# Performance work log

Hardware: AMD Instinct MI355X
Metric: run time of the kernel (lower is better)

Reference implementation:

```python
import jax, jax.numpy as jnp
import numpy as np

N_ATOMS = 100000
N_BONDS = 400000
ATOM_FDIM = 133
BOND_FDIM = 147
HIDDEN = 300
DEPTH = 3


def setup_inputs() -> dict:
    key = jax.random.key(0)
    ks = jax.random.split(key, 10)
    f_atoms = jax.random.normal(ks[0], (N_ATOMS, ATOM_FDIM), dtype=jnp.float32)
    f_bonds = jax.random.normal(ks[1], (N_BONDS, BOND_FDIM), dtype=jnp.float32)
    b2a = jax.random.randint(ks[2], (N_BONDS,), 0, N_ATOMS)
    b2revb = jax.random.randint(ks[3], (N_BONDS,), 0, N_BONDS)
    s_i = 1.0 / np.sqrt(BOND_FDIM)
    s_h = 1.0 / np.sqrt(HIDDEN)
    s_o = 1.0 / np.sqrt(ATOM_FDIM + HIDDEN)
    Wi_w = jax.random.uniform(ks[4], (HIDDEN, BOND_FDIM), jnp.float32, -s_i, s_i)
    Wi_b = jax.random.uniform(ks[5], (HIDDEN,), jnp.float32, -s_i, s_i)
    Wh_w = jax.random.uniform(ks[6], (HIDDEN, HIDDEN), jnp.float32, -s_h, s_h)
    Wh_b = jax.random.uniform(ks[7], (HIDDEN,), jnp.float32, -s_h, s_h)
    Wo_w = jax.random.uniform(ks[8], (HIDDEN, ATOM_FDIM + HIDDEN), jnp.float32, -s_o, s_o)
    Wo_b = jax.random.uniform(ks[9], (HIDDEN,), jnp.float32, -s_o, s_o)
    return {"f_atoms": f_atoms, "f_bonds": f_bonds, "b2a": b2a, "b2revb": b2revb,
            "Wi_w": Wi_w, "Wi_b": Wi_b, "Wh_w": Wh_w, "Wh_b": Wh_b,
            "Wo_w": Wo_w, "Wo_b": Wo_b}


def reference(f_atoms, f_bonds, b2a, b2revb, Wi_w, Wi_b, Wh_w, Wh_b, Wo_w, Wo_b):
    n_atoms = f_atoms.shape[0]
    # initial bond messages: [n_bonds, hidden]
    H_bonds = jax.nn.relu(f_bonds @ Wi_w.T + Wi_b)
    dest = b2a[b2revb]  # destination atom of each directed bond
    for _ in range(DEPTH - 1):
        # scatter-add bond messages onto destination atoms
        sum_msgs = jax.ops.segment_sum(H_bonds, dest, num_segments=n_atoms)
        # gather back to bonds from source atoms, subtract reverse-bond message
        msgs = sum_msgs[b2a] - H_bonds[b2revb]
        H_bonds = jax.nn.relu(H_bonds + msgs @ Wh_w.T + Wh_b)
    sum_msgs = jax.ops.segment_sum(H_bonds, dest, num_segments=n_atoms)
    H_atoms = jax.nn.relu(jnp.concatenate([f_atoms, sum_msgs], axis=1) @ Wo_w.T + Wo_b)
    return (H_atoms, H_bonds)
```

## Files before the change

kernel.cpp:

```cpp
#include <hip/hip_runtime.h>
#include <hip/hip_bf16.h>

#define NB 400000
#define NA 100000
#define AFD 133
#define BFD 147
#define HID 300
#define NP  320
#define SMP 304
#define NT  98

typedef short short8 __attribute__((ext_vector_type(8)));
typedef float f32x4 __attribute__((ext_vector_type(4)));

__device__ __forceinline__ ushort f2b(float f) {
    union { float f; unsigned u; } v; v.f = f;
    unsigned r = v.u + 0x7fffu + ((v.u >> 16) & 1u);
    return (ushort)(r >> 16);
}
__device__ __forceinline__ float b2f(ushort u) {
    union { unsigned u; float f; } v; v.u = ((unsigned)u) << 16;
    return v.f;
}

#define GLDS(gp, lp) __builtin_amdgcn_global_load_lds( \
    (const __attribute__((address_space(1))) void*)(gp), \
    (__attribute__((address_space(3))) void*)(lp), 16, 0, 0)


__global__ void pad_w_k(const float* __restrict__ W, ushort* __restrict__ Wp,
                        int N, int K, int Kp) {
    int idx = blockIdx.x * 256 + threadIdx.x;
    if (idx >= NP * Kp) return;
    int n = idx / Kp, k = idx - n * Kp;
    int t = k >> 5, kk = k & 31;
    int g = (kk & 15) >> 2, slot = (kk & 3) + ((kk >> 4) << 2);
    int gp = g ^ ((n >> 1) & 3);
    ushort v = (n < N && k < K) ? f2b(W[n * K + k]) : (ushort)0;
    Wp[(size_t)t * 10240 + n * 32 + gp * 8 + slot] = v;
}

__global__ void dest_k(const int* __restrict__ b2a, const int* __restrict__ b2revb,
                       int* __restrict__ dest) {
    int b = blockIdx.x * 256 + threadIdx.x;
    if (b < NB) dest[b] = b2a[b2revb[b]];
}

__global__ void count_k(const int* __restrict__ dest, int* __restrict__ cnt) {
    int b = blockIdx.x * 256 + threadIdx.x;
    if (b < NB) atomicAdd(&cnt[dest[b]], 1);
}

__global__ void scanA_k(const int* __restrict__ cnt, int* __restrict__ tsum) {
    __shared__ int sm[256];
    const int tid = threadIdx.x;
    int base = blockIdx.x * 1024 + tid * 4;
    int s = 0;
#pragma unroll
    for (int j = 0; j < 4; ++j) { int i = base + j; if (i < NA) s += cnt[i]; }
    sm[tid] = s; __syncthreads();
    for (int o = 128; o > 0; o >>= 1) {
        if (tid < o) sm[tid] += sm[tid + o];
        __syncthreads();
    }
    if (tid == 0) tsum[blockIdx.x] = sm[0];
}

__global__ void scanB_k(const int* __restrict__ tsum, int* __restrict__ toff,
                        int* __restrict__ rs) {
    if (threadIdx.x == 0) {
        int run = 0;
        for (int t = 0; t < NT; ++t) { toff[t] = run; run += tsum[t]; }
        rs[NA] = run;
    }
}

__global__ void scanC_k(const int* __restrict__ cnt, const int* __restrict__ toff,
                        int* __restrict__ rs) {
    __shared__ int sm[256];
    const int tid = threadIdx.x;
    int base = blockIdx.x * 1024 + tid * 4;
    int v[4]; int s = 0;
#pragma unroll
    for (int j = 0; j < 4; ++j) {
        v[j] = (base + j < NA) ? cnt[base + j] : 0;
        s += v[j];
    }
    sm[tid] = s; __syncthreads();
    for (int o = 1; o < 256; o <<= 1) {
        int x = (tid >= o) ? sm[tid - o] : 0;
        __syncthreads();
        sm[tid] += x;
        __syncthreads();
    }
    int acc = sm[tid] - s + toff[blockIdx.x];
#pragma unroll
    for (int j = 0; j < 4; ++j) {
        if (base + j < NA) rs[base + j] = acc;
        acc += v[j];
    }
}

__global__ void scatter_k(const int* __restrict__ dest, const int* __restrict__ rs,
                          int* __restrict__ cur, int* __restrict__ bl) {
    int b = blockIdx.x * 256 + threadIdx.x;
    if (b >= NB) return;
    int a = dest[b];
    int pos = rs[a] + atomicAdd(&cur[a], 1);
    bl[pos] = b;
}

template<int MODE, bool OUTF>
__global__ __launch_bounds__(512) void gemm_k(
    const float* __restrict__ F1, const float* __restrict__ Sum,
    const ushort* __restrict__ HbIn,
    const int* __restrict__ b2a, const int* __restrict__ b2revb,
    const ushort* __restrict__ W, const float* __restrict__ bias,
    ushort* __restrict__ Cb, float* __restrict__ Cf, int M)
{
    constexpr int KP = (MODE == 0) ? 192 : (MODE == 1) ? 320 : 448;
    constexpr int TILES = KP / 32;
    static_assert(KP % 64 == 0 && TILES % 2 == 0, "XOR swizzle needs 128B-mult rows, even tiles");
    __shared__ ushort As[128 * KP];
    __shared__ ushort Bs[2][320 * 32];

    const int tid = threadIdx.x;
    const int w = tid >> 6, lane = tid & 63;
    const int wr = w >> 2, wc = w & 3;
    const int g = lane >> 4, lr = lane & 15;
    const int m0 = blockIdx.x * 128;

    {
        const int row = tid >> 2, q = tid & 3;
        int grow = m0 + row;
        if (MODE == 2 && grow >= M) grow = M - 1;
        const int axw = (row & 7) << 4;
        char* abase = (char*)As + (size_t)row * (KP * 2);
        const float* sp = nullptr; const ushort* hp = nullptr;
        if (MODE == 1) {
            sp = Sum + (size_t)b2a[grow] * SMP;
            hp = HbIn + (size_t)b2revb[grow] * NP;
        }
#pragma unroll
        for (int t = 0; t < TILES; ++t) {
            const int k0 = t * 32 + 4 * q, k1 = k0 + 16;
            ushort o[8];
            if (MODE == 0) {
                const float* src = F1 + (size_t)grow * BFD;
#pragma unroll
                for (int s = 0; s < 4; ++s) o[s]     = (k0 + s < BFD) ? f2b(src[k0 + s]) : (ushort)0;
#pragma unroll
                for (int s = 0; s < 4; ++s) o[4 + s] = (k1 + s < BFD) ? f2b(src[k1 + s]) : (ushort)0;
            } else if (MODE == 1) {
                float4 s0 = *(const float4*)(sp + k0);
                float4 s1 = (k1 < SMP) ? *(const float4*)(sp + k1)
                                       : make_float4(0.f, 0.f, 0.f, 0.f);
                ushort4 h0 = *(const ushort4*)(hp + k0);
                ushort4 h1 = *(const ushort4*)(hp + k1);
                o[0] = f2b(s0.x - b2f(h0.x)); o[1] = f2b(s0.y - b2f(h0.y));
                o[2] = f2b(s0.z - b2f(h0.z)); o[3] = f2b(s0.w - b2f(h0.w));
                o[4] = f2b(s1.x - b2f(h1.x)); o[5] = f2b(s1.y - b2f(h1.y));
                o[6] = f2b(s1.z - b2f(h1.z)); o[7] = f2b(s1.w - b2f(h1.w));
            } else {
#pragma unroll
                for (int s = 0; s < 8; ++s) {
                    int k = (s < 4) ? (k0 + s) : (k1 + s - 4);
                    float x = 0.f;
                    if (k < AFD) x = F1[(size_t)grow * AFD + k];
                    else if (k < AFD + HID) x = Sum[(size_t)grow * SMP + (k - AFD)];
                    o[s] = f2b(x);
                }
            }
            ushort* dst = (ushort*)(abase + ((t * 64 + q * 16) ^ axw));
            *(ushort4*)dst       = make_ushort4(o[0], o[1], o[2], o[3]);
            *(ushort4*)(dst + 4) = make_ushort4(o[4], o[5], o[6], o[7]);
        }
    }

    auto stageB = [&](int t, int buf) {
        const ushort* wt = W + (size_t)t * 10240;
        ushort* bs = &Bs[buf][0];
        GLDS(wt + (size_t)w * 512 + lane * 8,        bs + w * 512);
        GLDS(wt + (size_t)(w + 8) * 512 + lane * 8,  bs + (w + 8) * 512);
        if (w < 4)
            GLDS(wt + (size_t)(w + 16) * 512 + lane * 8, bs + (w + 16) * 512);
    };

    f32x4 acc[4][5];
#pragma unroll
    for (int mi = 0; mi < 4; ++mi)
#pragma unroll
        for (int ni = 0; ni < 5; ++ni) acc[mi][ni] = (f32x4){0.f, 0.f, 0.f, 0.f};

    stageB(0, 0);
    __syncthreads();

    const int raxw = (lr & 7) << 4;
    const int bswz = ((lr >> 1) & 3);
    for (int t = 0; t < TILES; ++t) {
        if (t + 1 < TILES) stageB(t + 1, (t + 1) & 1);
        const ushort* bs = &Bs[t & 1][0];
        short8 af[4];
#pragma unroll
        for (int mi = 0; mi < 4; ++mi) {
            const int r = wr * 64 + mi * 16 + lr;
            af[mi] = *(const short8*)((const char*)As + (size_t)r * (KP * 2)
                                      + ((t * 64 + g * 16) ^ raxw));
        }
#pragma unroll
        for (int ni = 0; ni < 5; ++ni) {
            const int c = wc * 80 + ni * 16 + lr;
            short8 bf = *(const short8*)&bs[c * 32 + ((g ^ bswz) << 3)];
#pragma unroll
            for (int mi = 0; mi < 4; ++mi)
                acc[mi][ni] = __builtin_amdgcn_mfma_f32_16x16x32_bf16(af[mi], bf, acc[mi][ni], 0, 0, 0);
        }
        __syncthreads();
    }

#pragma unroll
    for (int ni = 0; ni < 5; ++ni) {
        const int col = wc * 80 + ni * 16 + lr;
        const float bv = (col < HID) ? bias[col] : 0.f;
#pragma unroll
        for (int mi = 0; mi < 4; ++mi) {
            const int row0 = m0 + wr * 64 + mi * 16 + g * 4;
#pragma unroll
            for (int r = 0; r < 4; ++r) {
                const int row = row0 + r;
                float v = acc[mi][ni][r] + bv;
                if (MODE == 1) v += b2f(HbIn[(size_t)row * NP + col]);
                v = fmaxf(v, 0.f);
                if (MODE == 2) {
                    if (col < HID && row < M) Cf[(size_t)row * HID + col] = v;
                } else {
                    Cb[(size_t)row * NP + col] = f2b(v);
                    if (OUTF && col < HID) Cf[(size_t)row * HID + col] = v;
                }
            }
        }
    }
}

__global__ void seg_sum_csr_k(const ushort* __restrict__ Hb, const int* __restrict__ rs,
                              const int* __restrict__ bl, float* __restrict__ sum) {
    int idx = blockIdx.x * 256 + threadIdx.x;
    if (idx >= NA * 38) return;
    int a = idx / 38, c = (idx - a * 38) * 8;
    int s0 = rs[a], s1 = rs[a + 1];
    float acc[8] = {0.f, 0.f, 0.f, 0.f, 0.f, 0.f, 0.f, 0.f};
    for (int j = s0; j < s1; ++j) {
        const ushort* p = &Hb[(size_t)bl[j] * NP + c];
        ushort4 u0 = *(const ushort4*)p, u1 = *(const ushort4*)(p + 4);
        acc[0] += b2f(u0.x); acc[1] += b2f(u0.y);
        acc[2] += b2f(u0.z); acc[3] += b2f(u0.w);
        acc[4] += b2f(u1.x); acc[5] += b2f(u1.y);
        acc[6] += b2f(u1.z); acc[7] += b2f(u1.w);
    }
    float* dst = &sum[(size_t)a * SMP + c];
    *(float4*)dst       = make_float4(acc[0], acc[1], acc[2], acc[3]);
    *(float4*)(dst + 4) = make_float4(acc[4], acc[5], acc[6], acc[7]);
}

extern "C" void kernel_launch(void* const* d_in, const int* in_sizes, int n_in,
                              void* d_out, int out_size, void* d_ws, size_t ws_size,
                              hipStream_t stream) {
    const float* f_atoms = (const float*)d_in[0];
    const float* f_bonds = (const float*)d_in[1];
    const int*   b2a     = (const int*)d_in[2];
    const int*   b2revb  = (const int*)d_in[3];
    const float* Wi_w    = (const float*)d_in[4];
    const float* Wi_b    = (const float*)d_in[5];
    const float* Wh_w    = (const float*)d_in[6];
    const float* Wh_b    = (const float*)d_in[7];
    const float* Wo_w    = (const float*)d_in[8];
    const float* Wo_b    = (const float*)d_in[9];
    float* out = (float*)d_out;

    char* ws = (char*)d_ws;
    ushort* HbA  = (ushort*)ws;            ws += (size_t)NB * NP * 2;
    ushort* HbB  = (ushort*)ws;            ws += (size_t)NB * NP * 2;
    float*  sum  = (float*)ws;             ws += (size_t)NA * SMP * 4;
    int*    dest = (int*)ws;               ws += (size_t)NB * 4;
    ushort* Wp0  = (ushort*)ws;            ws += (size_t)6  * 10240 * 2;
    ushort* Wp1  = (ushort*)ws;            ws += (size_t)10 * 10240 * 2;
    ushort* Wp2  = (ushort*)ws;            ws += (size_t)14 * 10240 * 2;
    int*    cnt  = (int*)ws;               ws += (size_t)NA * 4;
    int*    cur  = (int*)ws;               ws += (size_t)NA * 4;
    int*    rs   = (int*)ws;               ws += (size_t)(NA + 1) * 4;
    int*    bl   = (int*)ws;               ws += (size_t)NB * 4;
    int*    tsum = (int*)ws;               ws += 128 * 4;
    int*    toff = (int*)ws;               ws += 128 * 4;
    float* Hatoms = out;
    float* Hbonds = out + (size_t)NA * HID;

    pad_w_k<<<(NP * 192 + 255) / 256, 256, 0, stream>>>(Wi_w, Wp0, HID, BFD, 192);
    pad_w_k<<<(NP * NP  + 255) / 256, 256, 0, stream>>>(Wh_w, Wp1, HID, HID, NP);
    pad_w_k<<<(NP * 448 + 255) / 256, 256, 0, stream>>>(Wo_w, Wp2, HID, AFD + HID, 448);
    dest_k<<<(NB + 255) / 256, 256, 0, stream>>>(b2a, b2revb, dest);
    hipMemsetAsync(cnt, 0, (size_t)NA * 4, stream);
    hipMemsetAsync(cur, 0, (size_t)NA * 4, stream);
    count_k<<<(NB + 255) / 256, 256, 0, stream>>>(dest, cnt);
    scanA_k<<<NT, 256, 0, stream>>>(cnt, tsum);
    scanB_k<<<1, 64, 0, stream>>>(tsum, toff, rs);
    scanC_k<<<NT, 256, 0, stream>>>(cnt, toff, rs);
    scatter_k<<<(NB + 255) / 256, 256, 0, stream>>>(dest, rs, cur, bl);

    gemm_k<0, false><<<NB / 128, 512, 0, stream>>>(
        f_bonds, nullptr, nullptr, nullptr, nullptr, Wp0, Wi_b, HbA, nullptr, NB);

    seg_sum_csr_k<<<(NA * 38 + 255) / 256, 256, 0, stream>>>(HbA, rs, bl, sum);
    gemm_k<1, false><<<NB / 128, 512, 0, stream>>>(
        nullptr, sum, HbA, b2a, b2revb, Wp1, Wh_b, HbB, nullptr, NB);

    seg_sum_csr_k<<<(NA * 38 + 255) / 256, 256, 0, stream>>>(HbB, rs, bl, sum);
    gemm_k<1, true><<<NB / 128, 512, 0, stream>>>(
        nullptr, sum, HbB, b2a, b2revb, Wp1, Wh_b, HbA, Hbonds, NB);

    seg_sum_csr_k<<<(NA * 38 + 255) / 256, 256, 0, stream>>>(HbA, rs, bl, sum);
    gemm_k<2, false><<<(NA + 127) / 128, 512, 0, stream>>>(
        f_atoms, sum, nullptr, nullptr, nullptr, Wp2, Wo_b, nullptr, Hatoms, NA);
}
```

Measured before the change: 1.808 ms.

## Apply Wh before message passing and stream A tiles via direct-to-LDS loads

Uses linearity so that Y = H·Whᵀ is computed first, then segment-summed and gathered (sum_msgs·W − H_rev·W) in a separate elementwise update kernel, instead of building the gathered message matrix inside the GEMM prologue. The new H GEMM reads its A operand with global_load_lds double buffering like B, removing the gather from the GEMM. The change adds an extra Y buffer, an extra bf16 SY round-trip and another launch per iteration. Bf16 rounding now happens at different points, which may change accuracy. The K-slot layout of the packed weights is also changed to contiguous groups of 8.

```diff
diff --git a/kernel.cpp b/kernel.cpp
--- a/kernel.cpp
+++ b/kernel.cpp
@@ -34,10 +34,15 @@
     if (idx >= NP * Kp) return;
     int n = idx / Kp, k = idx - n * Kp;
     int t = k >> 5, kk = k & 31;
-    int g = (kk & 15) >> 2, slot = (kk & 3) + ((kk >> 4) << 2);
+    int g = kk >> 3, s = kk & 7;
     int gp = g ^ ((n >> 1) & 3);
     ushort v = (n < N && k < K) ? f2b(W[n * K + k]) : (ushort)0;
-    Wp[(size_t)t * 10240 + n * 32 + gp * 8 + slot] = v;
+    Wp[(size_t)t * 10240 + n * 32 + gp * 8 + s] = v;
+}
+
+__global__ void pad_bias_k(const float* __restrict__ bh, float* __restrict__ bhp) {
+    int i = blockIdx.x * 256 + threadIdx.x;
+    if (i < NP) bhp[i] = (i < HID) ? bh[i] : 0.f;
 }
 
 __global__ void dest_k(const int* __restrict__ b2a, const int* __restrict__ b2revb,
@@ -110,17 +115,15 @@
     bl[pos] = b;
 }
 
-template<int MODE, bool OUTF>
+template<int MODE>
 __global__ __launch_bounds__(512) void gemm_k(
     const float* __restrict__ F1, const float* __restrict__ Sum,
-    const ushort* __restrict__ HbIn,
-    const int* __restrict__ b2a, const int* __restrict__ b2revb,
     const ushort* __restrict__ W, const float* __restrict__ bias,
     ushort* __restrict__ Cb, float* __restrict__ Cf, int M)
 {
-    constexpr int KP = (MODE == 0) ? 192 : (MODE == 1) ? 320 : 448;
+    constexpr int KP = (MODE == 0) ? 192 : 448;
     constexpr int TILES = KP / 32;
-    static_assert(KP % 64 == 0 && TILES % 2 == 0, "XOR swizzle needs 128B-mult rows, even tiles");
+    static_assert(KP % 64 == 0 && TILES % 2 == 0, "XOR swizzle needs 128B rows, even tiles");
     __shared__ ushort As[128 * KP];
     __shared__ ushort Bs[2][320 * 32];
 
@@ -136,38 +139,22 @@
         if (MODE == 2 && grow >= M) grow = M - 1;
         const int axw = (row & 7) << 4;
         char* abase = (char*)As + (size_t)row * (KP * 2);
-        const float* sp = nullptr; const ushort* hp = nullptr;
-        if (MODE == 1) {
-            sp = Sum + (size_t)b2a[grow] * SMP;
-            hp = HbIn + (size_t)b2revb[grow] * NP;
-        }
 #pragma unroll
         for (int t = 0; t < TILES; ++t) {
-            const int k0 = t * 32 + 4 * q, k1 = k0 + 16;
+            const int k0 = t * 32 + q * 8;
             ushort o[8];
             if (MODE == 0) {
                 const float* src = F1 + (size_t)grow * BFD;
 #pragma unroll
-                for (int s = 0; s < 4; ++s) o[s]     = (k0 + s < BFD) ? f2b(src[k0 + s]) : (ushort)0;
-#pragma unroll
-                for (int s = 0; s < 4; ++s) o[4 + s] = (k1 + s < BFD) ? f2b(src[k1 + s]) : (ushort)0;
-            } else if (MODE == 1) {
-                float4 s0 = *(const float4*)(sp + k0);
-                float4 s1 = (k1 < SMP) ? *(const float4*)(sp + k1)
-                                       : make_float4(0.f, 0.f, 0.f, 0.f);
-                ushort4 h0 = *(const ushort4*)(hp + k0);
-                ushort4 h1 = *(const ushort4*)(hp + k1);
-                o[0] = f2b(s0.x - b2f(h0.x)); o[1] = f2b(s0.y - b2f(h0.y));
-                o[2] = f2b(s0.z - b2f(h0.z)); o[3] = f2b(s0.w - b2f(h0.w));
-                o[4] = f2b(s1.x - b2f(h1.x)); o[5] = f2b(s1.y - b2f(h1.y));
-                o[6] = f2b(s1.z - b2f(h1.z)); o[7] = f2b(s1.w - b2f(h1.w));
+                for (int s = 0; s < 8; ++s)
+                    o[s] = (k0 + s < BFD) ? f2b(src[k0 + s]) : (ushort)0;
             } else {
 #pragma unroll
                 for (int s = 0; s < 8; ++s) {
-                    int k = (s < 4) ? (k0 + s) : (k1 + s - 4);
+                    int k = k0 + s;
                     float x = 0.f;
                     if (k < AFD) x = F1[(size_t)grow * AFD + k];
-                    else if (k < AFD + HID) x = Sum[(size_t)grow * SMP + (k - AFD)];
+                    else if (k < AFD + SMP) x = Sum[(size_t)grow * SMP + (k - AFD)];
                     o[s] = f2b(x);
                 }
             }
@@ -196,7 +183,7 @@
     __syncthreads();
 
     const int raxw = (lr & 7) << 4;
-    const int bswz = ((lr >> 1) & 3);
+    const int bswz = (lr >> 1) & 3;
     for (int t = 0; t < TILES; ++t) {
         if (t + 1 < TILES) stageB(t + 1, (t + 1) & 1);
         const ushort* bs = &Bs[t & 1][0];
@@ -228,17 +215,136 @@
 #pragma unroll
             for (int r = 0; r < 4; ++r) {
                 const int row = row0 + r;
-                float v = acc[mi][ni][r] + bv;
-                if (MODE == 1) v += b2f(HbIn[(size_t)row * NP + col]);
-                v = fmaxf(v, 0.f);
+                float v = fmaxf(acc[mi][ni][r] + bv, 0.f);
                 if (MODE == 2) {
                     if (col < HID && row < M) Cf[(size_t)row * HID + col] = v;
                 } else {
                     Cb[(size_t)row * NP + col] = f2b(v);
-                    if (OUTF && col < HID) Cf[(size_t)row * HID + col] = v;
                 }
             }
         }
+    }
+}
+
+__global__ __launch_bounds__(512) void gemm_h_k(
+    const ushort* __restrict__ Hb, const ushort* __restrict__ W,
+    ushort* __restrict__ Y)
+{
+    __shared__ ushort As[2][4][128][8];
+    __shared__ ushort Bs[2][320 * 32];
+    const int tid = threadIdx.x;
+    const int w = tid >> 6, lane = tid & 63;
+    const int wr = w >> 2, wc = w & 3;
+    const int g = lane >> 4, lr = lane & 15;
+    const int m0 = blockIdx.x * 128;
+
+    const int q = w >> 1, r0 = (w & 1) * 64;
+    const ushort* aglob = Hb + (size_t)(m0 + r0 + lane) * NP + q * 8;
+
+    f32x4 acc[4][5];
+#pragma unroll
+    for (int mi = 0; mi < 4; ++mi)
+#pragma unroll
+        for (int ni = 0; ni < 5; ++ni) acc[mi][ni] = (f32x4){0.f, 0.f, 0.f, 0.f};
+
+    auto stageA = [&](int t, int buf) {
+        GLDS(aglob + t * 32, &As[buf][q][r0][0]);
+    };
+    auto stageB = [&](int t, int buf) {
+        const ushort* wt = W + (size_t)t * 10240;
+        ushort* bs = &Bs[buf][0];
+        GLDS(wt + (size_t)w * 512 + lane * 8,        bs + w * 512);
+        GLDS(wt + (size_t)(w + 8) * 512 + lane * 8,  bs + (w + 8) * 512);
+        if (w < 4)
+            GLDS(wt + (size_t)(w + 16) * 512 + lane * 8, bs + (w + 16) * 512);
+    };
+
+    stageA(0, 0); stageB(0, 0);
+    __syncthreads();
+
+    const int bswz = (lr >> 1) & 3;
+    for (int t = 0; t < 10; ++t) {
+        if (t < 9) { stageA(t + 1, (t + 1) & 1); stageB(t + 1, (t + 1) & 1); }
+        const int buf = t & 1;
+        short8 af[4];
+#pragma unroll
+        for (int mi = 0; mi < 4; ++mi)
+            af[mi] = *(const short8*)&As[buf][g][wr * 64 + mi * 16 + lr][0];
+#pragma unroll
+        for (int ni = 0; ni < 5; ++ni) {
+            const int c = wc * 80 + ni * 16 + lr;
+            short8 bf = *(const short8*)&Bs[buf][c * 32 + ((g ^ bswz) << 3)];
+#pragma unroll
+            for (int mi = 0; mi < 4; ++mi)
+                acc[mi][ni] = __builtin_amdgcn_mfma_f32_16x16x32_bf16(af[mi], bf, acc[mi][ni], 0, 0, 0);
+        }
+        __syncthreads();
+    }
+
+#pragma unroll
+    for (int ni = 0; ni < 5; ++ni) {
+        const int col = wc * 80 + ni * 16 + lr;
+#pragma unroll
+        for (int mi = 0; mi < 4; ++mi) {
+            const int row0 = m0 + wr * 64 + mi * 16 + g * 4;
+#pragma unroll
+            for (int r = 0; r < 4; ++r)
+                Y[(size_t)(row0 + r) * NP + col] = f2b(acc[mi][ni][r]);
+        }
+    }
+}
+
+__global__ void seg_sum_bf16_k(const ushort* __restrict__ Y, const int* __restrict__ rs,
+                               const int* __restrict__ bl, ushort* __restrict__ SY) {
+    int idx = blockIdx.x * 256 + threadIdx.x;
+    if (idx >= NA * 40) return;
+    int a = idx / 40, c = (idx - a * 40) * 8;
+    int s0 = rs[a], s1 = rs[a + 1];
+    float acc[8] = {0.f, 0.f, 0.f, 0.f, 0.f, 0.f, 0.f, 0.f};
+    for (int j = s0; j < s1; ++j) {
+        const ushort* p = &Y[(size_t)bl[j] * NP + c];
+        ushort4 u0 = *(const ushort4*)p, u1 = *(const ushort4*)(p + 4);
+        acc[0] += b2f(u0.x); acc[1] += b2f(u0.y);
+        acc[2] += b2f(u0.z); acc[3] += b2f(u0.w);
+        acc[4] += b2f(u1.x); acc[5] += b2f(u1.y);
+        acc[6] += b2f(u1.z); acc[7] += b2f(u1.w);
+    }
+    ushort* dst = &SY[(size_t)a * NP + c];
+    *(ushort4*)dst       = make_ushort4(f2b(acc[0]), f2b(acc[1]), f2b(acc[2]), f2b(acc[3]));
+    *(ushort4*)(dst + 4) = make_ushort4(f2b(acc[4]), f2b(acc[5]), f2b(acc[6]), f2b(acc[7]));
+}
+
+template<bool OUTF>
+__global__ void update_k(ushort* __restrict__ Hb, const ushort* __restrict__ SY,
+                         const ushort* __restrict__ Y,
+                         const int* __restrict__ b2a, const int* __restrict__ b2revb,
+                         const float* __restrict__ bhp, float* __restrict__ Hbonds) {
+    int idx = blockIdx.x * 256 + threadIdx.x;
+    if (idx >= NB * 40) return;
+    int b = idx / 40, c = (idx - b * 40) * 8;
+    int sa = b2a[b], rb = b2revb[b];
+    ushort* hp = &Hb[(size_t)b * NP + c];
+    const ushort* sp = &SY[(size_t)sa * NP + c];
+    const ushort* yp = &Y[(size_t)rb * NP + c];
+    ushort4 h0 = *(const ushort4*)hp,       h1 = *(const ushort4*)(hp + 4);
+    ushort4 s0 = *(const ushort4*)sp,       s1 = *(const ushort4*)(sp + 4);
+    ushort4 y0 = *(const ushort4*)yp,       y1 = *(const ushort4*)(yp + 4);
+    float4 bl0 = *(const float4*)&bhp[c], bl1 = *(const float4*)&bhp[c + 4];
+    float v[8];
+    v[0] = fmaxf(b2f(h0.x) + b2f(s0.x) - b2f(y0.x) + bl0.x, 0.f);
+    v[1] = fmaxf(b2f(h0.y) + b2f(s0.y) - b2f(y0.y) + bl0.y, 0.f);
+    v[2] = fmaxf(b2f(h0.z) + b2f(s0.z) - b2f(y0.z) + bl0.z, 0.f);
+    v[3] = fmaxf(b2f(h0.w) + b2f(s0.w) - b2f(y0.w) + bl0.w, 0.f);
+    v[4] = fmaxf(b2f(h1.x) + b2f(s1.x) - b2f(y1.x) + bl1.x, 0.f);
+    v[5] = fmaxf(b2f(h1.y) + b2f(s1.y) - b2f(y1.y) + bl1.y, 0.f);
+    v[6] = fmaxf(b2f(h1.z) + b2f(s1.z) - b2f(y1.z) + bl1.z, 0.f);
+    v[7] = fmaxf(b2f(h1.w) + b2f(s1.w) - b2f(y1.w) + bl1.w, 0.f);
+    *(ushort4*)hp       = make_ushort4(f2b(v[0]), f2b(v[1]), f2b(v[2]), f2b(v[3]));
+    *(ushort4*)(hp + 4) = make_ushort4(f2b(v[4]), f2b(v[5]), f2b(v[6]), f2b(v[7]));
+    if (OUTF && c < HID) {
+        float* op = &Hbonds[(size_t)b * HID + c];
+        *(float4*)op = make_float4(v[0], v[1], v[2], v[3]);
+        if (c + 4 < HID) *(float4*)(op + 4) = make_float4(v[4], v[5], v[6], v[7]);
     }
 }
 
@@ -278,13 +384,15 @@
     float* out = (float*)d_out;
 
     char* ws = (char*)d_ws;
-    ushort* HbA  = (ushort*)ws;            ws += (size_t)NB * NP * 2;
-    ushort* HbB  = (ushort*)ws;            ws += (size_t)NB * NP * 2;
+    ushort* Hb   = (ushort*)ws;            ws += (size_t)NB * NP * 2;
+    ushort* Y    = (ushort*)ws;            ws += (size_t)NB * NP * 2;
+    ushort* SY   = (ushort*)ws;            ws += (size_t)NA * NP * 2;
     float*  sum  = (float*)ws;             ws += (size_t)NA * SMP * 4;
     int*    dest = (int*)ws;               ws += (size_t)NB * 4;
     ushort* Wp0  = (ushort*)ws;            ws += (size_t)6  * 10240 * 2;
     ushort* Wp1  = (ushort*)ws;            ws += (size_t)10 * 10240 * 2;
     ushort* Wp2  = (ushort*)ws;            ws += (size_t)14 * 10240 * 2;
+    float*  bhp  = (float*)ws;             ws += (size_t)NP * 4;
     int*    cnt  = (int*)ws;               ws += (size_t)NA * 4;
     int*    cur  = (int*)ws;               ws += (size_t)NA * 4;
     int*    rs   = (int*)ws;               ws += (size_t)(NA + 1) * 4;
@@ -297,6 +405,7 @@
     pad_w_k<<<(NP * 192 + 255) / 256, 256, 0, stream>>>(Wi_w, Wp0, HID, BFD, 192);
     pad_w_k<<<(NP * NP  + 255) / 256, 256, 0, stream>>>(Wh_w, Wp1, HID, HID, NP);
     pad_w_k<<<(NP * 448 + 255) / 256, 256, 0, stream>>>(Wo_w, Wp2, HID, AFD + HID, 448);
+    pad_bias_k<<<2, 256, 0, stream>>>(Wh_b, bhp);
     dest_k<<<(NB + 255) / 256, 256, 0, stream>>>(b2a, b2revb, dest);
     hipMemsetAsync(cnt, 0, (size_t)NA * 4, stream);
     hipMemsetAsync(cur, 0, (size_t)NA * 4, stream);
@@ -306,18 +415,21 @@
     scanC_k<<<NT, 256, 0, stream>>>(cnt, toff, rs);
     scatter_k<<<(NB + 255) / 256, 256, 0, stream>>>(dest, rs, cur, bl);
 
-    gemm_k<0, false><<<NB / 128, 512, 0, stream>>>(
-        f_bonds, nullptr, nullptr, nullptr, nullptr, Wp0, Wi_b, HbA, nullptr, NB);
-
-    seg_sum_csr_k<<<(NA * 38 + 255) / 256, 256, 0, stream>>>(HbA, rs, bl, sum);
-    gemm_k<1, false><<<NB / 128, 512, 0, stream>>>(
-        nullptr, sum, HbA, b2a, b2revb, Wp1, Wh_b, HbB, nullptr, NB);
-
-    seg_sum_csr_k<<<(NA * 38 + 255) / 256, 256, 0, stream>>>(HbB, rs, bl, sum);
-    gemm_k<1, true><<<NB / 128, 512, 0, stream>>>(
-        nullptr, sum, HbB, b2a, b2revb, Wp1, Wh_b, HbA, Hbonds, NB);
-
-    seg_sum_csr_k<<<(NA * 38 + 255) / 256, 256, 0, stream>>>(HbA, rs, bl, sum);
-    gemm_k<2, false><<<(NA + 127) / 128, 512, 0, stream>>>(
-        f_atoms, sum, nullptr, nullptr, nullptr, Wp2, Wo_b, nullptr, Hatoms, NA);
-}
+    gemm_k<0><<<NB / 128, 512, 0, stream>>>(
+        f_bonds, nullptr, Wp0, Wi_b, Hb, nullptr, NB);
+
+    for (int it = 0; it < 2; ++it) {
+        gemm_h_k<<<NB / 128, 512, 0, stream>>>(Hb, Wp1, Y);
+        seg_sum_bf16_k<<<(NA * 40 + 255) / 256, 256, 0, stream>>>(Y, rs, bl, SY);
+        if (it == 0)
+            update_k<false><<<(NB * 40 + 255) / 256, 256, 0, stream>>>(
+                Hb, SY, Y, b2a, b2revb, bhp, nullptr);
+        else
+            update_k<true><<<(NB * 40 + 255) / 256, 256, 0, stream>>>(
+                Hb, SY, Y, b2a, b2revb, bhp, Hbonds);
+    }
+
+    seg_sum_csr_k<<<(NA * 38 + 255) / 256, 256, 0, stream>>>(Hb, rs, bl, sum);
+    gemm_k<2><<<(NA + 127) / 128, 512, 0, stream>>>(
+        f_atoms, sum, Wp2, Wo_b, nullptr, Hatoms, NA);
+}
```

Result: faster. 1.538 ms (-14.9%).
